# Kernel tuning notes

Measured on AMD Instinct MI355X. Metric: run time of the kernel, lower is better.

The kernel has to match this reference:

```python
import jax, jax.numpy as jnp
import numpy as np

CH = 512          # channels
HEADS = 8
HEAD_CH = 64
HIDDEN = HEADS * HEAD_CH  # 512
GROUPS = 32
EPS = 1e-5


def setup_inputs() -> dict:
    key = jax.random.key(0)
    ks = jax.random.split(key, 6)
    x = jax.random.normal(ks[0], (16, 32, 32, CH), dtype=jnp.float32)
    gn_scale = jnp.ones((CH,), dtype=jnp.float32)
    gn_offset = jnp.zeros((CH,), dtype=jnp.float32)
    w_qkv = jax.random.normal(ks[1], (CH, 3 * HIDDEN), dtype=jnp.float32) * 0.02
    # out_proj is zero-init in the original; use small random weights so the
    # residual branch is non-trivial for kernel correctness testing.
    w_out = jax.random.normal(ks[2], (HIDDEN, CH), dtype=jnp.float32) * 0.02
    b_out = jax.random.normal(ks[3], (CH,), dtype=jnp.float32) * 0.02
    return {"x": x, "gn_scale": gn_scale, "gn_offset": gn_offset,
            "w_qkv": w_qkv, "w_out": w_out, "b_out": b_out}


def group_norm(x, scale, offset):
    b, h, w, c = x.shape
    xg = x.reshape(b, h, w, GROUPS, c // GROUPS)
    mean = jnp.mean(xg, axis=(1, 2, 4), keepdims=True)
    var = jnp.var(xg, axis=(1, 2, 4), keepdims=True)
    xg = (xg - mean) * jax.lax.rsqrt(var + EPS)
    return xg.reshape(b, h, w, c) * scale + offset


def reference(x, gn_scale, gn_offset, w_qkv, w_out, b_out):
    b, h, w, c = x.shape
    n = h * w
    xn = jax.nn.silu(group_norm(x, gn_scale, gn_offset))
    qkv = jnp.einsum('bxyc,cd->bxyd', xn, w_qkv)  # [b,h,w,3*hidden]
    q, k, v = jnp.split(qkv, 3, axis=-1)
    # 'b x y (h c) -> b h c (x y)'
    def to_heads(a):
        a = a.reshape(b, n, HEADS, HEAD_CH)
        return jnp.transpose(a, (0, 2, 3, 1))  # b h d n
    q, k, v = to_heads(q), to_heads(k), to_heads(v)
    q = q * (HEAD_CH ** -0.5)
    sim = jnp.einsum('bhdi,bhdj->bhij', q, k)
    attn = jax.nn.softmax(sim, axis=-1)  # stable softmax (matches max-subtract)
    out = jnp.einsum('bhij,bhdj->bhid', attn, v)  # b h n d
    # 'b h (x y) d -> b x y (h d)'
    out = jnp.transpose(out, (0, 2, 1, 3)).reshape(b, h_ := h, w, HIDDEN) if False else \
          jnp.transpose(out, (0, 2, 1, 3)).reshape(b, h, w, HIDDEN)
    out = jnp.einsum('bxyd,dc->bxyc', out, w_out) + b_out
    return out + x
```

## Files before the change

### kernel.cpp

```cpp
#include <hip/hip_runtime.h>

#define BATCH 16
#define NPIX 1024
#define CH 512
#define HEADS 8
#define HD 64
#define GROUPS 32
#define CG 16
#define QKVW 1536

using bf16x8 = __attribute__((ext_vector_type(8))) short;
using f32x4  = __attribute__((ext_vector_type(4))) float;
using f32x16 = __attribute__((ext_vector_type(16))) float;

#if __has_builtin(__builtin_amdgcn_exp2f)
#define FEXP2 __builtin_amdgcn_exp2f
#else
#define FEXP2 exp2f
#endif

__device__ inline unsigned short f2bf(float f) {
  unsigned int u = __builtin_bit_cast(unsigned int, f);
  u += 0x7fffu + ((u >> 16) & 1u);
  return (unsigned short)(u >> 16);
}

__device__ inline unsigned cvtpk(float lo, float hi) {
  unsigned r;
  asm("v_cvt_pk_bf16_f32 %0, %1, %2" : "=v"(r) : "v"(lo), "v"(hi));
  return r;
}

__device__ inline bf16x8 lds_frag(const unsigned short* S, int row, int slot) {
  return *(const bf16x8*)(S + row * 64 + (((slot ^ (row & 7)) << 3)));
}

__device__ inline void gload16(const unsigned short* g, unsigned short* l) {
  __builtin_amdgcn_global_load_lds(
      (const __attribute__((address_space(1))) unsigned int*)g,
      (__attribute__((address_space(3))) unsigned int*)l, 16, 0, 0);
}

__global__ __launch_bounds__(256) void wconv_kernel(
    const float* __restrict__ src, unsigned short* __restrict__ dst,
    const int K, const int N, const int q_cols) {
  __shared__ float tile[64][65];
  const int nb = N >> 6;
  const int k0 = (blockIdx.x / nb) << 6, n0 = (blockIdx.x % nb) << 6;
  const int t = threadIdx.x;
  const int row = t >> 2, c0 = (t & 3) << 4;
#pragma unroll
  for (int j = 0; j < 4; ++j) {
    const float4 v = *reinterpret_cast<const float4*>(
        src + (size_t)(k0 + row) * N + n0 + c0 + j * 4);
    tile[row][c0 + j * 4 + 0] = v.x;
    tile[row][c0 + j * 4 + 1] = v.y;
    tile[row][c0 + j * 4 + 2] = v.z;
    tile[row][c0 + j * 4 + 3] = v.w;
  }
  __syncthreads();
  const int n = t >> 2, kc = (t & 3) << 4;
  const float s = ((n0 + n) < q_cols) ? (0.125f * 1.44269504f) : 1.f;
#pragma unroll
  for (int j = 0; j < 4; ++j) {
    ushort4 o;
    o.x = f2bf(tile[kc + j * 4 + 0][n] * s);
    o.y = f2bf(tile[kc + j * 4 + 1][n] * s);
    o.z = f2bf(tile[kc + j * 4 + 2][n] * s);
    o.w = f2bf(tile[kc + j * 4 + 3][n] * s);
    *reinterpret_cast<ushort4*>(dst + (size_t)(n0 + n) * K + k0 + kc + j * 4) = o;
  }
}

__global__ __launch_bounds__(256) void gn_silu_kernel(
    const float* __restrict__ x, const float* __restrict__ sc,
    const float* __restrict__ of, unsigned short* __restrict__ y) {
  const int b = blockIdx.x >> 5, g = blockIdx.x & 31;
  const size_t base = (size_t)b * NPIX * CH + (size_t)g * CG;
  const int t = threadIdx.x;

  float4 vv[16];
  float sum = 0.f, ssq = 0.f;
#pragma unroll
  for (int it = 0; it < 16; ++it) {
    const int e4 = t + 256 * it;
    const int p = e4 >> 2, c = (e4 & 3) * 4;
    vv[it] = *reinterpret_cast<const float4*>(x + base + (size_t)p * CH + c);
    sum += vv[it].x + vv[it].y + vv[it].z + vv[it].w;
    ssq += vv[it].x * vv[it].x + vv[it].y * vv[it].y +
           vv[it].z * vv[it].z + vv[it].w * vv[it].w;
  }
#pragma unroll
  for (int m = 32; m > 0; m >>= 1) {
    sum += __shfl_down(sum, m);
    ssq += __shfl_down(ssq, m);
  }
  __shared__ float rs[4], rq[4], mv[2];
  const int lane = t & 63, wid = t >> 6;
  if (lane == 0) { rs[wid] = sum; rq[wid] = ssq; }
  __syncthreads();
  if (t == 0) {
    const float s = rs[0] + rs[1] + rs[2] + rs[3];
    const float q = rq[0] + rq[1] + rq[2] + rq[3];
    const float mean = s * (1.f / 16384.f);
    const float var = q * (1.f / 16384.f) - mean * mean;
    mv[0] = mean;
    mv[1] = rsqrtf(var + 1e-5f);
  }
  __syncthreads();
  const float mean = mv[0], rstd = mv[1];

#pragma unroll
  for (int it = 0; it < 16; ++it) {
    const int e4 = t + 256 * it;
    const int p = e4 >> 2, c = (e4 & 3) * 4;
    const float4 s4 = *reinterpret_cast<const float4*>(sc + g * CG + c);
    const float4 o4 = *reinterpret_cast<const float4*>(of + g * CG + c);
    float r[4];
    r[0] = (vv[it].x - mean) * rstd * s4.x + o4.x;
    r[1] = (vv[it].y - mean) * rstd * s4.y + o4.y;
    r[2] = (vv[it].z - mean) * rstd * s4.z + o4.z;
    r[3] = (vv[it].w - mean) * rstd * s4.w + o4.w;
    ushort4 o;
    o.x = f2bf(r[0] / (1.f + __expf(-r[0])));
    o.y = f2bf(r[1] / (1.f + __expf(-r[1])));
    o.z = f2bf(r[2] / (1.f + __expf(-r[2])));
    o.w = f2bf(r[3] / (1.f + __expf(-r[3])));
    *reinterpret_cast<ushort4*>(y + base + (size_t)p * CH + c) = o;
  }
}

template <bool EPI>
__global__ __launch_bounds__(256) void gemm_bf16_kernel(
    const unsigned short* __restrict__ A, const unsigned short* __restrict__ BT,
    void* __restrict__ Cv, const int M, const int N,
    const float* __restrict__ bias, const float* __restrict__ resid,
    unsigned short* __restrict__ vT) {
  __shared__ unsigned short lds[16384];
  unsigned short* As = lds;
  unsigned short* Bs = lds + 8192;
  const int Kd = 512;
  const int t = threadIdx.x;
  int bid = blockIdx.x;
  { const int q = gridDim.x >> 3; bid = (bid & 7) * q + (bid >> 3); }
  const int nb = N >> 7;
  const int m0 = (bid / nb) << 7, n0 = (bid % nb) << 7;
  const int wv = t >> 6, lane = t & 63;
  const int wr = (wv >> 1) << 6, wc = (wv & 1) << 6;
  const int l15 = lane & 15, l4 = lane >> 4;
  const bool vmode = !EPI && (n0 >= 1024);

  const int srow = t >> 3, sslot = t & 7;
  const int gslot = sslot ^ (srow & 7);
  const unsigned short* ag = A + (size_t)(m0 + srow) * Kd + gslot * 8;
  const unsigned short* bg = BT + (size_t)(n0 + srow) * Kd + gslot * 8;
  unsigned short* aw = As + wv * 512;
  unsigned short* bw = Bs + wv * 512;

  f32x4 acc[4][4];
#pragma unroll
  for (int i = 0; i < 4; ++i)
#pragma unroll
    for (int j = 0; j < 4; ++j) acc[i][j] = {0.f, 0.f, 0.f, 0.f};

#pragma unroll
  for (int s = 0; s < 8; ++s) {
    const int k0 = s * 64;
#pragma unroll
    for (int i = 0; i < 4; ++i) {
      gload16(ag + (size_t)(32 * i) * Kd + k0, aw + i * 2048);
      gload16(bg + (size_t)(32 * i) * Kd + k0, bw + i * 2048);
    }
    __syncthreads();
#pragma unroll
    for (int kk = 0; kk < 2; ++kk) {
      bf16x8 af[4], bfr[4];
#pragma unroll
      for (int i = 0; i < 4; ++i) {
        af[i] = lds_frag(As, wr + i * 16 + l15, kk * 4 + l4);
        bfr[i] = lds_frag(Bs, wc + i * 16 + l15, kk * 4 + l4);
      }
      if (vmode) {
#pragma unroll
        for (int ni = 0; ni < 4; ++ni)
#pragma unroll
          for (int mi = 0; mi < 4; ++mi)
            acc[ni][mi] = __builtin_amdgcn_mfma_f32_16x16x32_bf16(
                bfr[ni], af[mi], acc[ni][mi], 0, 0, 0);
      } else {
#pragma unroll
        for (int mi = 0; mi < 4; ++mi)
#pragma unroll
          for (int ni = 0; ni < 4; ++ni)
            acc[mi][ni] = __builtin_amdgcn_mfma_f32_16x16x32_bf16(
                af[mi], bfr[ni], acc[mi][ni], 0, 0, 0);
      }
    }
    __syncthreads();
  }

  if (EPI) {
#pragma unroll
    for (int mi = 0; mi < 4; ++mi)
#pragma unroll
      for (int ni = 0; ni < 4; ++ni) {
        const int col = n0 + wc + ni * 16 + l15;
#pragma unroll
        for (int r = 0; r < 4; ++r) {
          const int row = m0 + wr + mi * 16 + l4 * 4 + r;
          const size_t idx = (size_t)row * N + col;
          ((float*)Cv)[idx] = acc[mi][ni][r] + bias[col] + resid[idx];
        }
      }
  } else {
    unsigned short* Ct = lds;
#pragma unroll
    for (int ii = 0; ii < 4; ++ii)
#pragma unroll
      for (int jj = 0; jj < 4; ++jj) {
        const int rb = vmode ? (wc + ii * 16 + l4 * 4) : (wr + ii * 16 + l4 * 4);
        const int col = vmode ? (wr + jj * 16 + l15) : (wc + jj * 16 + l15);
#pragma unroll
        for (int r = 0; r < 4; ++r) {
          const int row = rb + r;
          Ct[row * 128 + ((((col >> 3) ^ (row & 15))) << 3) + (col & 7)] =
              f2bf(acc[ii][jj][r]);
        }
      }
    __syncthreads();
    const int erow = t >> 4;
    const int eslot = t & 15;
    if (!vmode) {
#pragma unroll
      for (int j = 0; j < 8; ++j) {
        const int row = erow + 16 * j;
        const uint4 v = *reinterpret_cast<const uint4*>(
            Ct + row * 128 + ((eslot ^ (row & 15)) << 3));
        *reinterpret_cast<uint4*>(
            (unsigned short*)Cv + (size_t)(m0 + row) * N + n0 + eslot * 8) = v;
      }
    } else {
      const int bb = m0 >> 10;
#pragma unroll
      for (int j = 0; j < 8; ++j) {
        const int row = erow + 16 * j;
        const uint4 v = *reinterpret_cast<const uint4*>(
            Ct + row * 128 + ((eslot ^ (row & 15)) << 3));
        *reinterpret_cast<uint4*>(
            vT + (((size_t)(bb * 512 + (n0 - 1024) + row)) << 10) +
            (m0 & 1023) + eslot * 8) = v;
      }
    }
  }
}

__global__ __launch_bounds__(256) void attn_mfma_kernel(
    const unsigned short* __restrict__ qkv, const unsigned short* __restrict__ vT,
    unsigned short* __restrict__ outb) {
  __shared__ unsigned short Ks[2][64 * 64];
  __shared__ unsigned short Vt[2][64 * 64];

  int bid = blockIdx.x;
  { const int q = gridDim.x >> 3; bid = (bid & 7) * q + (bid >> 3); }
  const int qt = bid & 7, h = (bid >> 3) & 7, b = bid >> 6;
  const int t = threadIdx.x, wv = t >> 6, lane = t & 63;
  const int l31 = lane & 31, hi = lane >> 5;
  const int q0 = qt * 128 + wv * 32;
  const size_t base = (size_t)b * NPIX * QKVW + h * HD;

  bf16x8 qf[4];
#pragma unroll
  for (int dk = 0; dk < 4; ++dk)
    qf[dk] = *reinterpret_cast<const bf16x8*>(
        qkv + base + (size_t)(q0 + l31) * QKVW + dk * 16 + hi * 8);

  int off[2][4];
#pragma unroll
  for (int a = 0; a < 2; ++a)
#pragma unroll
    for (int c = 0; c < 4; ++c)
      off[a][c] = (a * 32 + l31) * 64 + (((c * 2 + hi) ^ (l31 & 7)) << 3);

  f32x16 oacc[2];
#pragma unroll
  for (int i = 0; i < 2; ++i)
#pragma unroll
    for (int r = 0; r < 16; ++r) oacc[i][r] = 0.f;
  float lrun = 0.f;

  const int srow = t >> 3, sslot = t & 7;
  const int gslot = sslot ^ (srow & 7);
  const unsigned short* kgp = qkv + base + 512 + (size_t)srow * QKVW + gslot * 8;
  const unsigned short* vgp =
      vT + (((size_t)(b * 512 + h * HD + srow)) << 10) + gslot * 8;
  unsigned short* kw[2] = {&Ks[0][0] + wv * 512, &Ks[1][0] + wv * 512};
  unsigned short* vw[2] = {&Vt[0][0] + wv * 512, &Vt[1][0] + wv * 512};

#pragma unroll
  for (int i = 0; i < 2; ++i) {
    gload16(kgp + (size_t)(32 * i) * QKVW, kw[0] + i * 2048);
    gload16(vgp + ((size_t)(32 * i) << 10), vw[0] + i * 2048);
    gload16(kgp + (size_t)(64 + 32 * i) * QKVW, kw[1] + i * 2048);
    gload16(vgp + ((size_t)(32 * i) << 10) + 64, vw[1] + i * 2048);
  }
  __syncthreads();

#pragma unroll
  for (int kt = 0; kt < 16; ++kt) {
    const int cur = kt & 1;
    const unsigned short* Kb = &Ks[cur][0];
    const unsigned short* Vb = &Vt[cur][0];

    f32x16 sacc[2];
#pragma unroll
    for (int i = 0; i < 2; ++i)
#pragma unroll
      for (int r = 0; r < 16; ++r) sacc[i][r] = 0.f;
    __builtin_amdgcn_s_setprio(1);
#pragma unroll
    for (int kb = 0; kb < 2; ++kb)
#pragma unroll
      for (int dk = 0; dk < 4; ++dk) {
        const bf16x8 kf = *(const bf16x8*)(Kb + off[kb][dk]);
        sacc[kb] = __builtin_amdgcn_mfma_f32_32x32x16_bf16(
            kf, qf[dk], sacc[kb], 0, 0, 0);
      }
    __builtin_amdgcn_s_setprio(0);

    float rsum = 0.f;
#pragma unroll
    for (int kb = 0; kb < 2; ++kb)
#pragma unroll
      for (int r = 0; r < 16; ++r) {
        sacc[kb][r] = FEXP2(sacc[kb][r]);
        rsum += sacc[kb][r];
      }
    {
      unsigned ru = __builtin_bit_cast(unsigned, rsum), rw = ru;
      asm("v_permlane32_swap_b32 %0, %1" : "+v"(ru), "+v"(rw));
      lrun += __builtin_bit_cast(float, ru) + __builtin_bit_cast(float, rw);
    }

    bf16x8 pf[4];
#pragma unroll
    for (int kk = 0; kk < 4; ++kk) {
      const int kb = kk >> 1, ra = (kk & 1) << 3;
      unsigned u = cvtpk(sacc[kb][ra + 0], sacc[kb][ra + 1]);
      unsigned w = cvtpk(sacc[kb][ra + 4], sacc[kb][ra + 5]);
      unsigned v = cvtpk(sacc[kb][ra + 2], sacc[kb][ra + 3]);
      unsigned x = cvtpk(sacc[kb][ra + 6], sacc[kb][ra + 7]);
      asm("v_permlane32_swap_b32 %0, %1" : "+v"(u), "+v"(w));
      asm("v_permlane32_swap_b32 %0, %1" : "+v"(v), "+v"(x));
      uint4 pw = {u, v, w, x};
      pf[kk] = __builtin_bit_cast(bf16x8, pw);
    }

    __builtin_amdgcn_s_setprio(1);
#pragma unroll
    for (int db = 0; db < 2; ++db)
#pragma unroll
      for (int kk = 0; kk < 4; ++kk) {
        const bf16x8 vf = *(const bf16x8*)(Vb + off[db][kk]);
        oacc[db] = __builtin_amdgcn_mfma_f32_32x32x16_bf16(
            vf, pf[kk], oacc[db], 0, 0, 0);
      }
    __builtin_amdgcn_s_setprio(0);

    __syncthreads();

    if (kt < 14) {
      const int n0n = (kt + 2) * 64;
#pragma unroll
      for (int i = 0; i < 2; ++i) {
        gload16(kgp + (size_t)(n0n + 32 * i) * QKVW, kw[cur] + i * 2048);
        gload16(vgp + ((size_t)(32 * i) << 10) + n0n, vw[cur] + i * 2048);
      }
    }
  }

  const float inv = 1.f / lrun;
  const size_t n = (size_t)b * NPIX + q0 + l31;
#pragma unroll
  for (int db = 0; db < 2; ++db)
#pragma unroll
    for (int rq = 0; rq < 4; ++rq) {
      uint2 o;
      o.x = cvtpk(oacc[db][rq * 4 + 0] * inv, oacc[db][rq * 4 + 1] * inv);
      o.y = cvtpk(oacc[db][rq * 4 + 2] * inv, oacc[db][rq * 4 + 3] * inv);
      *reinterpret_cast<uint2*>(
          outb + n * CH + h * HD + db * 32 + rq * 8 + hi * 4) = o;
    }
}

extern "C" void kernel_launch(void* const* d_in, const int* in_sizes, int n_in,
                              void* d_out, int out_size, void* d_ws, size_t ws_size,
                              hipStream_t stream) {
  const float* x = (const float*)d_in[0];
  const float* gsc = (const float*)d_in[1];
  const float* gof = (const float*)d_in[2];
  const float* wqkv = (const float*)d_in[3];
  const float* wout = (const float*)d_in[4];
  const float* bout = (const float*)d_in[5];
  float* out = (float*)d_out;

  unsigned short* qkvb = (unsigned short*)d_ws;
  unsigned short* xnb = qkvb + (size_t)16384 * 1536;
  unsigned short* wqT = xnb + (size_t)16384 * 512;
  unsigned short* woT = wqT + (size_t)1536 * 512;
  unsigned short* vTb = woT + (size_t)512 * 512;
  const size_t need = ((size_t)16384 * 1536 + (size_t)16384 * 512 +
                       (size_t)1536 * 512 + (size_t)512 * 512 +
                       (size_t)16 * 512 * 1024) * 2;
  if (ws_size < need) return;

  wconv_kernel<<<(512 / 64) * (1536 / 64), 256, 0, stream>>>(
      wqkv, wqT, 512, 1536, 512);
  wconv_kernel<<<(512 / 64) * (512 / 64), 256, 0, stream>>>(
      wout, woT, 512, 512, 0);
  gn_silu_kernel<<<BATCH * GROUPS, 256, 0, stream>>>(x, gsc, gof, xnb);
  gemm_bf16_kernel<false><<<(16384 / 128) * (1536 / 128), 256, 0, stream>>>(
      xnb, wqT, qkvb, 16384, 1536, nullptr, nullptr, vTb);
  attn_mfma_kernel<<<BATCH * HEADS * 8, 256, 0, stream>>>(qkvb, vTb, xnb);
  gemm_bf16_kernel<true><<<(16384 / 128) * (512 / 128), 256, 0, stream>>>(
      xnb, woT, out, 16384, 512, bout, x, nullptr);
}
```

Before: 133.9 us.

## Double-buffer GEMM LDS tiles with K-step 32 to overlap loads and MFMA

```diff
diff --git a/kernel.cpp b/kernel.cpp
--- a/kernel.cpp
+++ b/kernel.cpp
@@ -29,10 +29,6 @@
   unsigned r;
   asm("v_cvt_pk_bf16_f32 %0, %1, %2" : "=v"(r) : "v"(lo), "v"(hi));
   return r;
-}
-
-__device__ inline bf16x8 lds_frag(const unsigned short* S, int row, int slot) {
-  return *(const bf16x8*)(S + row * 64 + (((slot ^ (row & 7)) << 3)));
 }
 
 __device__ inline void gload16(const unsigned short* g, unsigned short* l) {
@@ -137,8 +133,6 @@
     const float* __restrict__ bias, const float* __restrict__ resid,
     unsigned short* __restrict__ vT) {
   __shared__ unsigned short lds[16384];
-  unsigned short* As = lds;
-  unsigned short* Bs = lds + 8192;
   const int Kd = 512;
   const int t = threadIdx.x;
   int bid = blockIdx.x;
@@ -150,12 +144,20 @@
   const int l15 = lane & 15, l4 = lane >> 4;
   const bool vmode = !EPI && (n0 >= 1024);
 
-  const int srow = t >> 3, sslot = t & 7;
-  const int gslot = sslot ^ (srow & 7);
+  const int srow = t >> 2, sslot = t & 3;
+  const int gslot = sslot ^ (srow & 3);
   const unsigned short* ag = A + (size_t)(m0 + srow) * Kd + gslot * 8;
   const unsigned short* bg = BT + (size_t)(n0 + srow) * Kd + gslot * 8;
-  unsigned short* aw = As + wv * 512;
-  unsigned short* bw = Bs + wv * 512;
+  unsigned short* Ab[2] = {lds, lds + 8192};
+  unsigned short* Bb[2] = {lds + 4096, lds + 12288};
+
+  const int fsw = (l4 ^ (l15 & 3)) << 3;
+  int offA[4], offB[4];
+#pragma unroll
+  for (int i = 0; i < 4; ++i) {
+    offA[i] = (wr + i * 16 + l15) * 32 + fsw;
+    offB[i] = (wc + i * 16 + l15) * 32 + fsw;
+  }
 
   f32x4 acc[4][4];
 #pragma unroll
@@ -164,37 +166,45 @@
     for (int j = 0; j < 4; ++j) acc[i][j] = {0.f, 0.f, 0.f, 0.f};
 
 #pragma unroll
-  for (int s = 0; s < 8; ++s) {
-    const int k0 = s * 64;
+  for (int i = 0; i < 2; ++i) {
+    gload16(ag + (size_t)(64 * i) * Kd, Ab[0] + wv * 512 + i * 2048);
+    gload16(bg + (size_t)(64 * i) * Kd, Bb[0] + wv * 512 + i * 2048);
+  }
+  __syncthreads();
+
+#pragma unroll
+  for (int s = 0; s < 16; ++s) {
+    const int cur = s & 1;
+    if (s < 15) {
+      const int k0 = (s + 1) * 32;
+#pragma unroll
+      for (int i = 0; i < 2; ++i) {
+        gload16(ag + (size_t)(64 * i) * Kd + k0,
+                Ab[cur ^ 1] + wv * 512 + i * 2048);
+        gload16(bg + (size_t)(64 * i) * Kd + k0,
+                Bb[cur ^ 1] + wv * 512 + i * 2048);
+      }
+    }
+    bf16x8 af[4], bfr[4];
 #pragma unroll
     for (int i = 0; i < 4; ++i) {
-      gload16(ag + (size_t)(32 * i) * Kd + k0, aw + i * 2048);
-      gload16(bg + (size_t)(32 * i) * Kd + k0, bw + i * 2048);
-    }
-    __syncthreads();
-#pragma unroll
-    for (int kk = 0; kk < 2; ++kk) {
-      bf16x8 af[4], bfr[4];
-#pragma unroll
-      for (int i = 0; i < 4; ++i) {
-        af[i] = lds_frag(As, wr + i * 16 + l15, kk * 4 + l4);
-        bfr[i] = lds_frag(Bs, wc + i * 16 + l15, kk * 4 + l4);
-      }
-      if (vmode) {
+      af[i] = *(const bf16x8*)(Ab[cur] + offA[i]);
+      bfr[i] = *(const bf16x8*)(Bb[cur] + offB[i]);
+    }
+    if (vmode) {
+#pragma unroll
+      for (int ni = 0; ni < 4; ++ni)
+#pragma unroll
+        for (int mi = 0; mi < 4; ++mi)
+          acc[ni][mi] = __builtin_amdgcn_mfma_f32_16x16x32_bf16(
+              bfr[ni], af[mi], acc[ni][mi], 0, 0, 0);
+    } else {
+#pragma unroll
+      for (int mi = 0; mi < 4; ++mi)
 #pragma unroll
         for (int ni = 0; ni < 4; ++ni)
-#pragma unroll
-          for (int mi = 0; mi < 4; ++mi)
-            acc[ni][mi] = __builtin_amdgcn_mfma_f32_16x16x32_bf16(
-                bfr[ni], af[mi], acc[ni][mi], 0, 0, 0);
-      } else {
-#pragma unroll
-        for (int mi = 0; mi < 4; ++mi)
-#pragma unroll
-          for (int ni = 0; ni < 4; ++ni)
-            acc[mi][ni] = __builtin_amdgcn_mfma_f32_16x16x32_bf16(
-                af[mi], bfr[ni], acc[mi][ni], 0, 0, 0);
-      }
+          acc[mi][ni] = __builtin_amdgcn_mfma_f32_16x16x32_bf16(
+              af[mi], bfr[ni], acc[mi][ni], 0, 0, 0);
     }
     __syncthreads();
   }
```

Measured after the change: 136.7 us. 2.1% more time.
